# Kernel optimization log

Measured on AMD Instinct MI355X. Metric: run time of the kernel, lower is better.

The kernel has to match this reference:

```python
import jax, jax.numpy as jnp
import numpy as np

B, TQ, TKV, D, H = 4, 1024, 2048, 1024, 16
DH = D // H


def setup_inputs() -> dict:
    key = jax.random.key(0)
    ks = jax.random.split(key, 12)
    s = 0.02
    return {
        "x": jax.random.normal(ks[0], (B, TQ, D), jnp.float32),
        "k_cache": jax.random.normal(ks[1], (B, TKV, D), jnp.float32),
        "v_cache": jax.random.normal(ks[2], (B, TKV, D), jnp.float32),
        "mask": jnp.zeros((TQ, TKV), jnp.float32),  # additive attention bias
        "Wq": jax.random.normal(ks[3], (D, D), jnp.float32) * s,
        "bq": jax.random.normal(ks[4], (D,), jnp.float32) * s,
        "Wk": jax.random.normal(ks[5], (D, D), jnp.float32) * s,  # key: no bias (Whisper-style)
        "Wv": jax.random.normal(ks[6], (D, D), jnp.float32) * s,
        "bv": jax.random.normal(ks[7], (D,), jnp.float32) * s,
        "Wo": jax.random.normal(ks[8], (D, D), jnp.float32) * s,
        "bo": jax.random.normal(ks[9], (D,), jnp.float32) * s,
    }


def reference(x, k_cache, v_cache, mask, Wq, bq, Wk, Wv, bv, Wo, bo):
    b, tq, d = x.shape
    scale = (d // H) ** -0.25
    # QKV projections (torch Linear: y = x @ W.T + b)
    q = x @ Wq.T + bq                      # [B,Tq,D]
    k_new = x @ Wk.T                       # [B,Tq,D] (key has no bias)
    v_new = x @ Wv.T + bv                  # [B,Tq,D]
    # KV-cache append: write last Tq positions
    k_cache = k_cache.at[:, -tq:, :].set(k_new)
    v_cache = v_cache.at[:, -tq:, :].set(v_new)
    # split heads
    qh = q.reshape(b, tq, H, DH) * scale           # [B,Tq,H,Dh]
    kh = k_cache.reshape(b, -1, H, DH) * scale     # [B,Tkv,H,Dh]
    vh = v_cache.reshape(b, -1, H, DH)             # [B,Tkv,H,Dh]
    qk = jnp.einsum("bqhd,bkhd->bhqk", qh, kh) + mask  # [B,H,Tq,Tkv]
    w = jax.nn.softmax(qk.astype(jnp.float32), axis=-1).astype(qh.dtype)
    wv = jnp.einsum("bhqk,bkhd->bqhd", w, vh).reshape(b, tq, d)
    out = wv @ Wo.T + bo
    return out, k_cache, v_cache
```

## Files before the change

### kernel.cpp

```cpp
#include <hip/hip_runtime.h>
#include <hip/hip_bf16.h>


typedef __bf16 bf16_t;
typedef __attribute__((ext_vector_type(4))) float f32x4;
typedef __attribute__((ext_vector_type(8))) __bf16 bf16x8;
typedef __attribute__((ext_vector_type(4))) __bf16 bf16x4;
typedef __attribute__((ext_vector_type(4))) unsigned short u16x4;

__device__ inline bf16x4 cvt4(float4 f) {
    bf16x4 o;
    o.x = (bf16_t)f.x; o.y = (bf16_t)f.y; o.z = (bf16_t)f.z; o.w = (bf16_t)f.w;
    return o;
}

__device__ inline void gload_lds16(const void* g, void* s) {
    __builtin_amdgcn_global_load_lds(
        (const __attribute__((address_space(1))) void*)g,
        (__attribute__((address_space(3))) void*)s, 16, 0, 0);
}

__device__ inline bf16x8 ldsr128(const bf16_t* p) {
    bf16x8 d;
    unsigned a = (unsigned)(size_t)(const __attribute__((address_space(3))) bf16_t*)p;
    asm volatile("ds_read_b128 %0, %1" : "=v"(d) : "v"(a));
    return d;
}

#define WAIT_LGKM0 do { asm volatile("s_waitcnt lgkmcnt(0)" ::: "memory"); \
                        __builtin_amdgcn_sched_barrier(0); } while (0)
#define WAIT_VM(n) asm volatile("s_waitcnt vmcnt(" #n ")" ::: "memory")

__device__ inline unsigned cvt_pk_bf16(float lo, float hi) {
    unsigned r;
    asm("v_cvt_pk_bf16_f32 %0, %1, %2" : "=v"(r) : "v"(lo), "v"(hi));
    return r;
}
__device__ inline void pswap32(unsigned& a, unsigned& b) {
    asm("v_permlane32_swap_b32 %0, %1" : "+v"(a), "+v"(b));
}
__device__ inline void pswap16(unsigned& a, unsigned& b) {
    asm("v_permlane16_swap_b32 %0, %1" : "+v"(a), "+v"(b));
}

#if __has_builtin(__builtin_amdgcn_exp2f)
__device__ inline float exp2_fast(float x) { return __builtin_amdgcn_exp2f(x); }
#else
__device__ inline float exp2_fast(float x) { return exp2f(x); }
#endif


__global__ void cast_f32_bf16_k(const float* __restrict__ src, bf16_t* __restrict__ dst, int n4) {
    int i = blockIdx.x * blockDim.x + threadIdx.x;
    if (i >= n4) return;
    float4 f = reinterpret_cast<const float4*>(src)[i];
    reinterpret_cast<bf16x4*>(dst)[i] = cvt4(f);
}

__global__ void build_wqkv_k(const float* __restrict__ Wq, const float* __restrict__ Wk,
                             const float* __restrict__ Wv, bf16_t* __restrict__ dst) {
    int i = blockIdx.x * blockDim.x + threadIdx.x;
    if (i >= 786432) return;
    int e0 = i * 4;
    int row = e0 >> 10;
    const float* src;
    if (row < 1024)       src = Wq + e0;
    else if (row < 2048)  src = Wk + (e0 - 1048576);
    else                  src = Wv + (e0 - 2097152);
    float4 f = *reinterpret_cast<const float4*>(src);
    reinterpret_cast<bf16x4*>(dst)[i] = cvt4(f);
}

__global__ void build_bias_k(const float* __restrict__ bq, const float* __restrict__ bv,
                             float* __restrict__ bias) {
    int i = blockIdx.x * blockDim.x + threadIdx.x;
    if (i >= 3072) return;
    float v;
    if (i < 1024)      v = bq[i];
    else if (i < 2048) v = 0.f;
    else               v = bv[i - 2048];
    bias[i] = v;
}

__global__ void copy_old2_k(const float* __restrict__ kc, const float* __restrict__ vc,
                            float* __restrict__ kout, float* __restrict__ vout,
                            bf16_t* __restrict__ k_bf) {
    int i = blockIdx.x * blockDim.x + threadIdx.x;
    if (i >= 2097152) return;
    int which = i >> 20;
    int ii = i & 1048575;
    int b = ii >> 18;
    int r = ii & 262143;
    size_t off = (size_t)b * 2097152 + (size_t)r * 4;
    if (which == 0) {
        float4 f = *reinterpret_cast<const float4*>(kc + off);
        *reinterpret_cast<float4*>(kout + off) = f;
        reinterpret_cast<bf16x4*>(k_bf + off)[0] = cvt4(f);
    } else {
        float4 f = *reinterpret_cast<const float4*>(vc + off);
        *reinterpret_cast<float4*>(vout + off) = f;
    }
}

__global__ __launch_bounds__(256) void transpose_v_k(const float* __restrict__ vout,
                                                     bf16_t* __restrict__ vT) {
    __shared__ bf16_t t[64][65];
    int blk = blockIdx.x;
    int kvt = blk >> 6;
    int bh  = blk & 63;
    int b = bh >> 4, h = bh & 15;
    int kv0 = kvt * 64;
    int tid = threadIdx.x;
    int c = tid & 63, r0 = tid >> 6;
    #pragma unroll
    for (int rr = r0; rr < 64; rr += 4)
        t[rr][c] = (bf16_t)vout[((size_t)b * 2048 + kv0 + rr) * 1024 + h * 64 + c];
    __syncthreads();
    #pragma unroll
    for (int dd = r0; dd < 64; dd += 4)
        vT[((size_t)bh * 64 + dd) * 2048 + kv0 + c] = t[c][dd];
}

__global__ void mask_bf16_k(const float* __restrict__ mask, bf16_t* __restrict__ maskB) {
    int i = blockIdx.x * blockDim.x + threadIdx.x;
    if (i >= 2097152) return;
    int r   = i & 3;
    int c16 = (i >> 2) & 15;
    int qd  = (i >> 6) & 3;
    int kb  = (i >> 8) & 127;
    int qb  = i >> 15;
    float v = mask[(size_t)(qb * 16 + c16) * 2048 + kb * 16 + qd * 4 + r] * 1.4426950408889634f;
    maskB[i] = (bf16_t)v;
}

__global__ __launch_bounds__(512, 2) void gemm8_k(const bf16_t* __restrict__ A,
                                                  const bf16_t* __restrict__ Bw,
                                                  const float* __restrict__ bias,
                                                  bf16_t* __restrict__ q_bf,
                                                  float* __restrict__ kout,
                                                  bf16_t* __restrict__ k_bf,
                                                  float* __restrict__ vout) {
    const int K = 1024;
    __shared__ __align__(16) bf16_t As[2][16384];
    __shared__ __align__(16) bf16_t Bs[2][16384];
    int flat = blockIdx.y * 16 + blockIdx.x;
    int logi = (flat & 7) * 24 + (flat >> 3);
    int m0 = (logi / 12) * 256, n0 = (logi % 12) * 256;
    int tid = threadIdx.x;
    int lane = tid & 63, w = tid >> 6;
    int wrM = w >> 2, wrN = w & 3;
    int col16 = lane & 15, quad = lane >> 4;
    int cx = (quad ^ (col16 & 7)) * 8;

    int sr = tid >> 3;
    int scb = ((tid & 7) ^ (sr & 7)) * 8;
    const bf16_t* ga = A + (size_t)(m0 + sr) * K + scb;
    const bf16_t* gb = Bw + (size_t)(n0 + sr) * K + scb;
    int ldst = sr * 64 + (tid & 7) * 8;

    auto stageA = [&](int d, int kt) {
        size_t ko = (size_t)kt * 64;
        gload_lds16(ga + ko, &As[d][ldst]);
        gload_lds16(ga + 64 * (size_t)K + ko, &As[d][ldst + 4096]);
        gload_lds16(ga + 128 * (size_t)K + ko, &As[d][ldst + 8192]);
        gload_lds16(ga + 192 * (size_t)K + ko, &As[d][ldst + 12288]);
    };
    auto stageB = [&](int d, int kt) {
        size_t ko = (size_t)kt * 64;
        gload_lds16(gb + ko, &Bs[d][ldst]);
        gload_lds16(gb + 64 * (size_t)K + ko, &Bs[d][ldst + 4096]);
        gload_lds16(gb + 128 * (size_t)K + ko, &Bs[d][ldst + 8192]);
        gload_lds16(gb + 192 * (size_t)K + ko, &Bs[d][ldst + 12288]);
    };

    int arow = wrM * 128 + col16;
    int brow = wrN * 64 + col16;

    f32x4 zero = {0.f, 0.f, 0.f, 0.f};
    f32x4 acc[8][4];
    #pragma unroll
    for (int mi = 0; mi < 8; mi++)
        #pragma unroll
        for (int ni = 0; ni < 4; ni++) acc[mi][ni] = zero;

    stageA(0, 0);
    stageB(0, 0);
    stageA(1, 1);
    WAIT_VM(4);
    __builtin_amdgcn_s_barrier();

    for (int kt = 0; kt < 16; kt++) {
        int d = kt & 1;
        const bf16_t* Ad = As[d];
        const bf16_t* Bd = Bs[d];
        bf16x8 a0[4][2], bb0[2][2];
        #pragma unroll
        for (int mi = 0; mi < 4; mi++) {
            const bf16_t* p = &Ad[(arow + mi * 16) * 64];
            a0[mi][0] = ldsr128(p + cx);
            a0[mi][1] = ldsr128(p + (cx ^ 32));
        }
        #pragma unroll
        for (int ni = 0; ni < 2; ni++) {
            const bf16_t* p = &Bd[(brow + ni * 16) * 64];
            bb0[ni][0] = ldsr128(p + cx);
            bb0[ni][1] = ldsr128(p + (cx ^ 32));
        }
        if (kt < 15) stageB(d ^ 1, kt + 1);
        __builtin_amdgcn_s_barrier();
        WAIT_LGKM0;
        __builtin_amdgcn_s_setprio(1);
        #pragma unroll
        for (int mi = 0; mi < 4; mi++)
            #pragma unroll
            for (int ni = 0; ni < 2; ni++) {
                acc[mi][ni] = __builtin_amdgcn_mfma_f32_16x16x32_bf16(a0[mi][0], bb0[ni][0], acc[mi][ni], 0, 0, 0);
                acc[mi][ni] = __builtin_amdgcn_mfma_f32_16x16x32_bf16(a0[mi][1], bb0[ni][1], acc[mi][ni], 0, 0, 0);
            }
        __builtin_amdgcn_s_setprio(0);
        __builtin_amdgcn_s_barrier();
        bf16x8 bb1[2][2];
        #pragma unroll
        for (int ni = 0; ni < 2; ni++) {
            const bf16_t* p = &Bd[(brow + 32 + ni * 16) * 64];
            bb1[ni][0] = ldsr128(p + cx);
            bb1[ni][1] = ldsr128(p + (cx ^ 32));
        }
        __builtin_amdgcn_s_barrier();
        WAIT_LGKM0;
        __builtin_amdgcn_s_setprio(1);
        #pragma unroll
        for (int mi = 0; mi < 4; mi++)
            #pragma unroll
            for (int ni = 0; ni < 2; ni++) {
                acc[mi][ni + 2] = __builtin_amdgcn_mfma_f32_16x16x32_bf16(a0[mi][0], bb1[ni][0], acc[mi][ni + 2], 0, 0, 0);
                acc[mi][ni + 2] = __builtin_amdgcn_mfma_f32_16x16x32_bf16(a0[mi][1], bb1[ni][1], acc[mi][ni + 2], 0, 0, 0);
            }
        __builtin_amdgcn_s_setprio(0);
        __builtin_amdgcn_s_barrier();
        bf16x8 a1[4][2];
        #pragma unroll
        for (int mi = 0; mi < 4; mi++) {
            const bf16_t* p = &Ad[(arow + 64 + mi * 16) * 64];
            a1[mi][0] = ldsr128(p + cx);
            a1[mi][1] = ldsr128(p + (cx ^ 32));
        }
        __builtin_amdgcn_s_barrier();
        WAIT_LGKM0;
        __builtin_amdgcn_s_setprio(1);
        #pragma unroll
        for (int mi = 0; mi < 4; mi++)
            #pragma unroll
            for (int ni = 0; ni < 2; ni++) {
                acc[mi + 4][ni] = __builtin_amdgcn_mfma_f32_16x16x32_bf16(a1[mi][0], bb0[ni][0], acc[mi + 4][ni], 0, 0, 0);
                acc[mi + 4][ni] = __builtin_amdgcn_mfma_f32_16x16x32_bf16(a1[mi][1], bb0[ni][1], acc[mi + 4][ni], 0, 0, 0);
            }
        __builtin_amdgcn_s_setprio(0);
        __builtin_amdgcn_s_barrier();
        if (kt < 14) {
            stageA(d, kt + 2);
            WAIT_VM(4);
        } else {
            WAIT_VM(0);
        }
        __builtin_amdgcn_s_barrier();
        __builtin_amdgcn_s_setprio(1);
        #pragma unroll
        for (int mi = 0; mi < 4; mi++)
            #pragma unroll
            for (int ni = 0; ni < 2; ni++) {
                acc[mi + 4][ni + 2] = __builtin_amdgcn_mfma_f32_16x16x32_bf16(a1[mi][0], bb1[ni][0], acc[mi + 4][ni + 2], 0, 0, 0);
                acc[mi + 4][ni + 2] = __builtin_amdgcn_mfma_f32_16x16x32_bf16(a1[mi][1], bb1[ni][1], acc[mi + 4][ni + 2], 0, 0, 0);
            }
        __builtin_amdgcn_s_setprio(0);
        __builtin_amdgcn_s_barrier();
    }

    int mb = m0 + wrM * 128 + quad * 4;
    int nb = n0 + wrN * 64 + col16;
    if (n0 < 1024) {
        #pragma unroll
        for (int ni = 0; ni < 4; ni++) {
            int gn = nb + ni * 16;
            float bia = bias[gn];
            #pragma unroll
            for (int mi = 0; mi < 8; mi++) {
                int gm = mb + mi * 16;
                #pragma unroll
                for (int r = 0; r < 4; r++)
                    q_bf[(size_t)(gm + r) * 1024 + gn] = (bf16_t)(acc[mi][ni][r] + bia);
            }
        }
    } else if (n0 < 2048) {
        #pragma unroll
        for (int ni = 0; ni < 4; ni++) {
            int gn = nb + ni * 16;
            float bia = bias[gn];
            int n2 = gn - 1024;
            #pragma unroll
            for (int mi = 0; mi < 8; mi++) {
                int gm = mb + mi * 16;
                #pragma unroll
                for (int r = 0; r < 4; r++) {
                    int gmr = gm + r;
                    int b = gmr >> 10, t = gmr & 1023;
                    size_t off = ((size_t)b * 2048 + 1024 + t) * 1024 + n2;
                    float v = acc[mi][ni][r] + bia;
                    kout[off] = v;
                    k_bf[off] = (bf16_t)v;
                }
            }
        }
    } else {
        #pragma unroll
        for (int ni = 0; ni < 4; ni++) {
            int gn = nb + ni * 16;
            float bia = bias[gn];
            int n2 = gn - 2048;
            #pragma unroll
            for (int mi = 0; mi < 8; mi++) {
                int gm = mb + mi * 16;
                #pragma unroll
                for (int r = 0; r < 4; r++) {
                    int gmr = gm + r;
                    int b = gmr >> 10, t = gmr & 1023;
                    vout[((size_t)b * 2048 + 1024 + t) * 1024 + n2] = acc[mi][ni][r] + bia;
                }
            }
        }
    }
}

__global__ __launch_bounds__(256) void gemm_wo_k(const bf16_t* __restrict__ A,
                                                 const bf16_t* __restrict__ Bw,
                                                 const float* __restrict__ bias,
                                                 float* __restrict__ out0) {
    const int K = 1024;
    __shared__ __align__(16) bf16_t As[2][4096];
    __shared__ __align__(16) bf16_t Bs[2][4096];
    int m0 = blockIdx.x * 128, n0 = blockIdx.y * 128;
    int tid = threadIdx.x;
    int lane = tid & 63, w = tid >> 6;
    int wr = w >> 1, wc = w & 1;
    int col16 = lane & 15, quad = lane >> 4;

    int srow = tid >> 2;
    int scol = ((tid & 3) ^ ((srow >> 1) & 3)) * 8;
    const bf16_t* ga = A + (size_t)(m0 + srow) * K + scol;
    const bf16_t* gb = Bw + (size_t)(n0 + srow) * K + scol;

    int qsw = (quad ^ ((col16 >> 1) & 3)) * 8;

    f32x4 zero = {0.f, 0.f, 0.f, 0.f};
    f32x4 acc[4][4];
    #pragma unroll
    for (int mi = 0; mi < 4; mi++)
        #pragma unroll
        for (int ni = 0; ni < 4; ni++) acc[mi][ni] = zero;

    auto stageg = [&](int d, int k) {
        gload_lds16(ga + k, &As[d][tid * 8]);
        gload_lds16(ga + (size_t)64 * K + k, &As[d][tid * 8 + 2048]);
        gload_lds16(gb + k, &Bs[d][tid * 8]);
        gload_lds16(gb + (size_t)64 * K + k, &Bs[d][tid * 8 + 2048]);
    };

    stageg(0, 0);
    __syncthreads();
    for (int kb = 0; kb < 32; kb++) {
        int cur = kb & 1;
        if (kb < 31) stageg(cur ^ 1, (kb + 1) * 32);
        bf16x8 af[4], bfr[4];
        #pragma unroll
        for (int mi = 0; mi < 4; mi++)
            af[mi] = ldsr128(&As[cur][(wr * 64 + mi * 16 + col16) * 32 + qsw]);
        #pragma unroll
        for (int ni = 0; ni < 4; ni++)
            bfr[ni] = ldsr128(&Bs[cur][(wc * 64 + ni * 16 + col16) * 32 + qsw]);
        WAIT_LGKM0;
        #pragma unroll
        for (int mi = 0; mi < 4; mi++)
            #pragma unroll
            for (int ni = 0; ni < 4; ni++)
                acc[mi][ni] = __builtin_amdgcn_mfma_f32_16x16x32_bf16(
                    af[mi], bfr[ni], acc[mi][ni], 0, 0, 0);
        __syncthreads();
    }

    int mbase = m0 + wr * 64 + quad * 4;
    int nbase = n0 + wc * 64 + col16;
    #pragma unroll
    for (int ni = 0; ni < 4; ni++) {
        int gn = nbase + ni * 16;
        float bia = bias[gn];
        #pragma unroll
        for (int mi = 0; mi < 4; mi++) {
            int gm = mbase + mi * 16;
            #pragma unroll
            for (int r = 0; r < 4; r++)
                out0[(size_t)(gm + r) * 1024 + gn] = acc[mi][ni][r] + bia;
        }
    }
}

__global__ __launch_bounds__(512, 4) void attn_k(const bf16_t* __restrict__ qbf,
                                                 const bf16_t* __restrict__ kbf,
                                                 const bf16_t* __restrict__ vT,
                                                 const bf16_t* __restrict__ maskB,
                                                 bf16_t* __restrict__ wv) {
    __shared__ __align__(16) bf16_t Ks[2][4096];
    __shared__ __align__(16) bf16_t Vs[2][4096];
    int logical = (blockIdx.x & 7) * 64 + (blockIdx.x >> 3);
    int bh = logical >> 3;
    int qtb = logical & 7;
    int b = bh >> 4, h = bh & 15;
    int tid = threadIdx.x, w = tid >> 6, lane = tid & 63;
    int col16 = lane & 15, quad = lane >> 4;
    int c7 = col16 & 7;
    int cx = (quad ^ c7) * 8;
    int qr0 = qtb * 128 + w * 16;

    int sr = tid >> 3, sc = (tid & 7) ^ ((tid >> 3) & 7);
    const bf16_t* kg = kbf + ((size_t)b * 2048 + sr) * 1024 + h * 64 + sc * 8;
    const bf16_t* vg = vT + ((size_t)bh * 64 + sr) * 2048 + sc * 8;
    auto stage = [&](int d, int kv0) {
        gload_lds16(kg + (size_t)kv0 * 1024, &Ks[d][tid * 8]);
        gload_lds16(vg + kv0, &Vs[d][tid * 8]);
    };

    const bf16_t* qrow = qbf + ((size_t)b * 1024 + qr0 + col16) * 1024 + h * 64;
    bf16x8 aq0 = *reinterpret_cast<const bf16x8*>(qrow + quad * 8);
    bf16x8 aq1 = *reinterpret_cast<const bf16x8*>(qrow + 32 + quad * 8);

    const bf16_t* mbase = maskB + (size_t)(qtb * 8 + w) * 32768 + quad * 64 + col16 * 4;

    f32x4 zero = {0.f, 0.f, 0.f, 0.f};
    f32x4 oacc[4];
    #pragma unroll
    for (int dt = 0; dt < 4; dt++) oacc[dt] = zero;
    float lrow = 0.f;

    stage(0, 0);
    __syncthreads();

    for (int t = 0; t < 32; t++) {
        int cur = t & 1;
        if (t < 31) stage(cur ^ 1, (t + 1) * 64);
        bf16x8 kf[4][2];
        #pragma unroll
        for (int nt = 0; nt < 4; nt++) {
            const bf16_t* kr = &Ks[cur][(nt * 16 + col16) * 64];
            kf[nt][0] = ldsr128(kr + cx);
            kf[nt][1] = ldsr128(kr + (cx ^ 32));
        }
        u16x4 m4[4];
        #pragma unroll
        for (int nt = 0; nt < 4; nt++)
            m4[nt] = *reinterpret_cast<const u16x4*>(mbase + (size_t)(t * 4 + nt) * 256);
        WAIT_LGKM0;
        f32x4 sv[4];
        __builtin_amdgcn_s_setprio(1);
        #pragma unroll
        for (int nt = 0; nt < 4; nt++) {
            sv[nt] = __builtin_amdgcn_mfma_f32_16x16x32_bf16(kf[nt][0], aq0, zero, 0, 0, 0);
            sv[nt] = __builtin_amdgcn_mfma_f32_16x16x32_bf16(kf[nt][1], aq1, sv[nt], 0, 0, 0);
        }
        __builtin_amdgcn_s_setprio(0);
        unsigned pk[4][2];
        #pragma unroll
        for (int nt = 0; nt < 4; nt++) {
            float p[4];
            #pragma unroll
            for (int r = 0; r < 4; r++) {
                float mv = __builtin_bit_cast(float, (unsigned)m4[nt][r] << 16);
                p[r] = exp2_fast(fmaf(sv[nt][r], 0.18033688011112042f, mv));
                lrow += p[r];
            }
            pk[nt][0] = cvt_pk_bf16(p[0], p[1]);
            pk[nt][1] = cvt_pk_bf16(p[2], p[3]);
        }
        union PB { unsigned u[4]; bf16x8 v; };
        PB pf0, pf1;
        {
            unsigned a0 = pk[0][0], b0 = pk[1][0];
            pswap32(a0, b0); pswap16(a0, b0);
            pf0.u[0] = a0; pf0.u[2] = b0;
            unsigned a1 = pk[0][1], b1 = pk[1][1];
            pswap32(a1, b1); pswap16(a1, b1);
            pf0.u[1] = a1; pf0.u[3] = b1;
            unsigned a2 = pk[2][0], b2 = pk[3][0];
            pswap32(a2, b2); pswap16(a2, b2);
            pf1.u[0] = a2; pf1.u[2] = b2;
            unsigned a3 = pk[2][1], b3 = pk[3][1];
            pswap32(a3, b3); pswap16(a3, b3);
            pf1.u[1] = a3; pf1.u[3] = b3;
        }
        bf16x8 vf[4][2];
        #pragma unroll
        for (int dt = 0; dt < 4; dt++) {
            const bf16_t* vr = &Vs[cur][(dt * 16 + col16) * 64];
            vf[dt][0] = ldsr128(vr + cx);
            vf[dt][1] = ldsr128(vr + (cx ^ 32));
        }
        WAIT_LGKM0;
        __builtin_amdgcn_s_setprio(1);
        #pragma unroll
        for (int dt = 0; dt < 4; dt++) {
            oacc[dt] = __builtin_amdgcn_mfma_f32_16x16x32_bf16(vf[dt][0], pf0.v, oacc[dt], 0, 0, 0);
            oacc[dt] = __builtin_amdgcn_mfma_f32_16x16x32_bf16(vf[dt][1], pf1.v, oacc[dt], 0, 0, 0);
        }
        __builtin_amdgcn_s_setprio(0);
        __syncthreads();
    }

    lrow += __shfl_xor(lrow, 16);
    lrow += __shfl_xor(lrow, 32);
    float inv = 1.f / lrow;
    bf16_t* orow = wv + ((size_t)b * 1024 + qr0 + col16) * 1024 + h * 64 + quad * 4;
    #pragma unroll
    for (int dt = 0; dt < 4; dt++) {
        bf16x4 o4;
        #pragma unroll
        for (int r = 0; r < 4; r++) o4[r] = (bf16_t)(oacc[dt][r] * inv);
        *reinterpret_cast<bf16x4*>(orow + dt * 16) = o4;
    }
}


extern "C" void kernel_launch(void* const* d_in, const int* in_sizes, int n_in,
                              void* d_out, int out_size, void* d_ws, size_t ws_size,
                              hipStream_t stream) {
    const float* x    = (const float*)d_in[0];
    const float* kc   = (const float*)d_in[1];
    const float* vc   = (const float*)d_in[2];
    const float* mask = (const float*)d_in[3];
    const float* Wq   = (const float*)d_in[4];
    const float* bq   = (const float*)d_in[5];
    const float* Wk   = (const float*)d_in[6];
    const float* Wv   = (const float*)d_in[7];
    const float* bv   = (const float*)d_in[8];
    const float* Wo   = (const float*)d_in[9];
    const float* bo   = (const float*)d_in[10];

    float* out0 = (float*)d_out;
    float* kout = out0 + 4194304;
    float* vout = out0 + 12582912;

    char* ws = (char*)d_ws;
    bf16_t* x_bf     = (bf16_t*)(ws);
    bf16_t* wqkv_bf  = (bf16_t*)(ws + 8388608);
    bf16_t* wo_bf    = (bf16_t*)(ws + 14680064);
    float*  bias_qkv = (float*)(ws + 16777216);
    bf16_t* q_bf     = (bf16_t*)(ws + 16789504);
    bf16_t* k_bf     = (bf16_t*)(ws + 25178112);
    bf16_t* vT_bf    = (bf16_t*)(ws + 41955328);
    bf16_t* wv_bf    = (bf16_t*)(ws + 58732544);
    bf16_t* maskB    = (bf16_t*)(ws + 67108864);

    cast_f32_bf16_k<<<4096, 256, 0, stream>>>(x, x_bf, 1048576);
    build_wqkv_k<<<3072, 256, 0, stream>>>(Wq, Wk, Wv, wqkv_bf);
    cast_f32_bf16_k<<<1024, 256, 0, stream>>>(Wo, wo_bf, 262144);
    build_bias_k<<<12, 256, 0, stream>>>(bq, bv, bias_qkv);
    mask_bf16_k<<<8192, 256, 0, stream>>>(mask, maskB);
    copy_old2_k<<<8192, 256, 0, stream>>>(kc, vc, kout, vout, k_bf);
    gemm8_k<<<dim3(16, 12), 512, 0, stream>>>(x_bf, wqkv_bf, bias_qkv,
                                              q_bf, kout, k_bf, vout);
    transpose_v_k<<<2048, 256, 0, stream>>>(vout, vT_bf);
    attn_k<<<512, 512, 0, stream>>>(q_bf, k_bf, vT_bf, maskB, wv_bf);
    gemm_wo_k<<<dim3(32, 8), 256, 0, stream>>>(wv_bf, wo_bf, bo, out0);
}
```

Before: 307.9 us.

## Fuse preprocessing kernels into one launch and split V transpose by cache region

Merges the six casting and copy kernels into a single block-dispatched prep kernel. It also moves the transpose of the old V-cache half into that kernel, reading directly from the input cache, so the post-GEMM transpose only handles the newly projected half. Nontemporal loads and stores are added on streaming copies and on GEMM epilogues to reduce cache pollution and launch overhead. The cost is a large heterogeneous kernel with branchy dispatch, and nontemporal stores on k_bf and q_bf may evict data that the attention kernel reads soon after.

Measured after the change: 317.0 us. +2.9%, slower.

```diff
diff --git a/kernel.cpp b/kernel.cpp
--- a/kernel.cpp
+++ b/kernel.cpp
@@ -4,11 +4,12 @@
 
 typedef __bf16 bf16_t;
 typedef __attribute__((ext_vector_type(4))) float f32x4;
+typedef __attribute__((ext_vector_type(4))) float f4v;
 typedef __attribute__((ext_vector_type(8))) __bf16 bf16x8;
 typedef __attribute__((ext_vector_type(4))) __bf16 bf16x4;
 typedef __attribute__((ext_vector_type(4))) unsigned short u16x4;
 
-__device__ inline bf16x4 cvt4(float4 f) {
+__device__ inline bf16x4 cvt4v(f4v f) {
     bf16x4 o;
     o.x = (bf16_t)f.x; o.y = (bf16_t)f.y; o.z = (bf16_t)f.z; o.w = (bf16_t)f.w;
     return o;
@@ -49,56 +50,83 @@
 __device__ inline float exp2_fast(float x) { return exp2f(x); }
 #endif
 
-
-__global__ void cast_f32_bf16_k(const float* __restrict__ src, bf16_t* __restrict__ dst, int n4) {
-    int i = blockIdx.x * blockDim.x + threadIdx.x;
-    if (i >= n4) return;
-    float4 f = reinterpret_cast<const float4*>(src)[i];
-    reinterpret_cast<bf16x4*>(dst)[i] = cvt4(f);
-}
-
-__global__ void build_wqkv_k(const float* __restrict__ Wq, const float* __restrict__ Wk,
-                             const float* __restrict__ Wv, bf16_t* __restrict__ dst) {
-    int i = blockIdx.x * blockDim.x + threadIdx.x;
-    if (i >= 786432) return;
-    int e0 = i * 4;
-    int row = e0 >> 10;
-    const float* src;
-    if (row < 1024)       src = Wq + e0;
-    else if (row < 2048)  src = Wk + (e0 - 1048576);
-    else                  src = Wv + (e0 - 2097152);
-    float4 f = *reinterpret_cast<const float4*>(src);
-    reinterpret_cast<bf16x4*>(dst)[i] = cvt4(f);
-}
-
-__global__ void build_bias_k(const float* __restrict__ bq, const float* __restrict__ bv,
-                             float* __restrict__ bias) {
-    int i = blockIdx.x * blockDim.x + threadIdx.x;
-    if (i >= 3072) return;
-    float v;
-    if (i < 1024)      v = bq[i];
-    else if (i < 2048) v = 0.f;
-    else               v = bv[i - 2048];
-    bias[i] = v;
-}
-
-__global__ void copy_old2_k(const float* __restrict__ kc, const float* __restrict__ vc,
-                            float* __restrict__ kout, float* __restrict__ vout,
-                            bf16_t* __restrict__ k_bf) {
-    int i = blockIdx.x * blockDim.x + threadIdx.x;
-    if (i >= 2097152) return;
-    int which = i >> 20;
-    int ii = i & 1048575;
-    int b = ii >> 18;
-    int r = ii & 262143;
-    size_t off = (size_t)b * 2097152 + (size_t)r * 4;
-    if (which == 0) {
-        float4 f = *reinterpret_cast<const float4*>(kc + off);
-        *reinterpret_cast<float4*>(kout + off) = f;
-        reinterpret_cast<bf16x4*>(k_bf + off)[0] = cvt4(f);
+__global__ __launch_bounds__(256) void prep_all_k(
+        const float* __restrict__ x, const float* __restrict__ kc,
+        const float* __restrict__ vc, const float* __restrict__ mask,
+        const float* __restrict__ Wq, const float* __restrict__ Wk,
+        const float* __restrict__ Wv, const float* __restrict__ Wo,
+        const float* __restrict__ bq, const float* __restrict__ bv,
+        bf16_t* __restrict__ x_bf, bf16_t* __restrict__ wqkv_bf,
+        bf16_t* __restrict__ wo_bf, float* __restrict__ bias,
+        bf16_t* __restrict__ maskB, float* __restrict__ kout,
+        float* __restrict__ vout, bf16_t* __restrict__ k_bf,
+        bf16_t* __restrict__ vT) {
+    __shared__ bf16_t tsh[64][65];
+    int blk = blockIdx.x, tid = threadIdx.x;
+    if (blk < 1024) {
+        int kvt = blk >> 6;
+        int bh  = blk & 63;
+        int b = bh >> 4, h = bh & 15;
+        int kv0 = kvt * 64;
+        int c = tid & 63, r0 = tid >> 6;
+        #pragma unroll
+        for (int rr = r0; rr < 64; rr += 4)
+            tsh[rr][c] = (bf16_t)vc[((size_t)b * 2048 + kv0 + rr) * 1024 + h * 64 + c];
+        __syncthreads();
+        #pragma unroll
+        for (int dd = r0; dd < 64; dd += 4)
+            vT[((size_t)bh * 64 + dd) * 2048 + kv0 + c] = tsh[c][dd];
+    } else if (blk < 9216) {
+        int i = (blk - 1024) * 256 + tid;
+        int which = i >> 20;
+        int ii = i & 1048575;
+        int b = ii >> 18;
+        int r = ii & 262143;
+        size_t off = (size_t)b * 2097152 + (size_t)r * 4;
+        if (which == 0) {
+            f4v f = __builtin_nontemporal_load(reinterpret_cast<const f4v*>(kc + off));
+            __builtin_nontemporal_store(f, reinterpret_cast<f4v*>(kout + off));
+            __builtin_nontemporal_store(cvt4v(f), reinterpret_cast<bf16x4*>(k_bf + off));
+        } else {
+            f4v f = *reinterpret_cast<const f4v*>(vc + off);
+            __builtin_nontemporal_store(f, reinterpret_cast<f4v*>(vout + off));
+        }
+    } else if (blk < 13312) {
+        int i = (blk - 9216) * 256 + tid;
+        f4v f = __builtin_nontemporal_load(reinterpret_cast<const f4v*>(x) + i);
+        reinterpret_cast<bf16x4*>(x_bf)[i] = cvt4v(f);
+    } else if (blk < 16384) {
+        int i = (blk - 13312) * 256 + tid;
+        int e0 = i * 4;
+        int row = e0 >> 10;
+        const float* src;
+        if (row < 1024)       src = Wq + e0;
+        else if (row < 2048)  src = Wk + (e0 - 1048576);
+        else                  src = Wv + (e0 - 2097152);
+        f4v f = __builtin_nontemporal_load(reinterpret_cast<const f4v*>(src));
+        reinterpret_cast<bf16x4*>(wqkv_bf)[i] = cvt4v(f);
+    } else if (blk < 24576) {
+        int i = (blk - 16384) * 256 + tid;
+        int r   = i & 3;
+        int c16 = (i >> 2) & 15;
+        int qd  = (i >> 6) & 3;
+        int kb  = (i >> 8) & 127;
+        int qb  = i >> 15;
+        float v = mask[(size_t)(qb * 16 + c16) * 2048 + kb * 16 + qd * 4 + r] * 1.4426950408889634f;
+        maskB[i] = (bf16_t)v;
+    } else if (blk < 25600) {
+        int i = (blk - 24576) * 256 + tid;
+        f4v f = __builtin_nontemporal_load(reinterpret_cast<const f4v*>(Wo) + i);
+        reinterpret_cast<bf16x4*>(wo_bf)[i] = cvt4v(f);
     } else {
-        float4 f = *reinterpret_cast<const float4*>(vc + off);
-        *reinterpret_cast<float4*>(vout + off) = f;
+        int i = (blk - 25600) * 256 + tid;
+        if (i < 3072) {
+            float v;
+            if (i < 1024)      v = bq[i];
+            else if (i < 2048) v = 0.f;
+            else               v = bv[i - 2048];
+            bias[i] = v;
+        }
     }
 }
 
@@ -109,7 +137,7 @@
     int kvt = blk >> 6;
     int bh  = blk & 63;
     int b = bh >> 4, h = bh & 15;
-    int kv0 = kvt * 64;
+    int kv0 = 1024 + kvt * 64;
     int tid = threadIdx.x;
     int c = tid & 63, r0 = tid >> 6;
     #pragma unroll
@@ -119,18 +147,6 @@
     #pragma unroll
     for (int dd = r0; dd < 64; dd += 4)
         vT[((size_t)bh * 64 + dd) * 2048 + kv0 + c] = t[c][dd];
-}
-
-__global__ void mask_bf16_k(const float* __restrict__ mask, bf16_t* __restrict__ maskB) {
-    int i = blockIdx.x * blockDim.x + threadIdx.x;
-    if (i >= 2097152) return;
-    int r   = i & 3;
-    int c16 = (i >> 2) & 15;
-    int qd  = (i >> 6) & 3;
-    int kb  = (i >> 8) & 127;
-    int qb  = i >> 15;
-    float v = mask[(size_t)(qb * 16 + c16) * 2048 + kb * 16 + qd * 4 + r] * 1.4426950408889634f;
-    maskB[i] = (bf16_t)v;
 }
 
 __global__ __launch_bounds__(512, 2) void gemm8_k(const bf16_t* __restrict__ A,
@@ -288,7 +304,8 @@
                 int gm = mb + mi * 16;
                 #pragma unroll
                 for (int r = 0; r < 4; r++)
-                    q_bf[(size_t)(gm + r) * 1024 + gn] = (bf16_t)(acc[mi][ni][r] + bia);
+                    __builtin_nontemporal_store((bf16_t)(acc[mi][ni][r] + bia),
+                                                &q_bf[(size_t)(gm + r) * 1024 + gn]);
             }
         }
     } else if (n0 < 2048) {
@@ -306,8 +323,8 @@
                     int b = gmr >> 10, t = gmr & 1023;
                     size_t off = ((size_t)b * 2048 + 1024 + t) * 1024 + n2;
                     float v = acc[mi][ni][r] + bia;
-                    kout[off] = v;
-                    k_bf[off] = (bf16_t)v;
+                    __builtin_nontemporal_store(v, &kout[off]);
+                    __builtin_nontemporal_store((bf16_t)v, &k_bf[off]);
                 }
             }
         }
@@ -324,7 +341,8 @@
                 for (int r = 0; r < 4; r++) {
                     int gmr = gm + r;
                     int b = gmr >> 10, t = gmr & 1023;
-                    vout[((size_t)b * 2048 + 1024 + t) * 1024 + n2] = acc[mi][ni][r] + bia;
+                    __builtin_nontemporal_store(acc[mi][ni][r] + bia,
+                        &vout[((size_t)b * 2048 + 1024 + t) * 1024 + n2]);
                 }
             }
         }
@@ -398,7 +416,8 @@
             int gm = mbase + mi * 16;
             #pragma unroll
             for (int r = 0; r < 4; r++)
-                out0[(size_t)(gm + r) * 1024 + gn] = acc[mi][ni][r] + bia;
+                __builtin_nontemporal_store(acc[mi][ni][r] + bia,
+                                            &out0[(size_t)(gm + r) * 1024 + gn]);
         }
     }
 }
@@ -557,15 +576,12 @@
     bf16_t* wv_bf    = (bf16_t*)(ws + 58732544);
     bf16_t* maskB    = (bf16_t*)(ws + 67108864);
 
-    cast_f32_bf16_k<<<4096, 256, 0, stream>>>(x, x_bf, 1048576);
-    build_wqkv_k<<<3072, 256, 0, stream>>>(Wq, Wk, Wv, wqkv_bf);
-    cast_f32_bf16_k<<<1024, 256, 0, stream>>>(Wo, wo_bf, 262144);
-    build_bias_k<<<12, 256, 0, stream>>>(bq, bv, bias_qkv);
-    mask_bf16_k<<<8192, 256, 0, stream>>>(mask, maskB);
-    copy_old2_k<<<8192, 256, 0, stream>>>(kc, vc, kout, vout, k_bf);
+    prep_all_k<<<25612, 256, 0, stream>>>(x, kc, vc, mask, Wq, Wk, Wv, Wo, bq, bv,
+                                          x_bf, wqkv_bf, wo_bf, bias_qkv, maskB,
+                                          kout, vout, k_bf, vT_bf);
     gemm8_k<<<dim3(16, 12), 512, 0, stream>>>(x_bf, wqkv_bf, bias_qkv,
                                               q_bf, kout, k_bf, vout);
-    transpose_v_k<<<2048, 256, 0, stream>>>(vout, vT_bf);
+    transpose_v_k<<<1024, 256, 0, stream>>>(vout, vT_bf);
     attn_k<<<512, 512, 0, stream>>>(q_bf, k_bf, vT_bf, maskB, wv_bf);
     gemm_wo_k<<<dim3(32, 8), 256, 0, stream>>>(wv_bf, wo_bf, bo, out0);
 }
```
